# Kernel optimization log

Measured on AMD Instinct MI355X. Metric: run time of the kernel, lower is better.

Reference implementation:

```python
import jax, jax.numpy as jnp
import numpy as np

# SLAYER SRM-alpha neuron constants (standard slayerPytorch yaml defaults)
THETA = 10.0      # spike threshold
TAU_SR = 10.0     # synaptic response time constant
TAU_REF = 1.0     # refractory time constant
SCALE_REF = 2.0   # refractory scale (kernel amplitude = -scaleRef*theta)
TS = 1.0          # simulation timestep
K_LEN = 100       # SRM kernel truncation length (kernel is negligible beyond this)
A_REF = float(np.exp(-TS / TAU_REF))
# refractory alpha kernel ref[m] = K_REF * m * A_REF**m  (= -scaleRef*theta*(m*Ts/tauRef)*exp(1-m*Ts/tauRef))
K_REF = -SCALE_REF * THETA * float(np.e) * (TS / TAU_REF)


def _srm_kernel():
    # eps(t) = (t/tauSr) * exp(1 - t/tauSr), eps(0) = 0
    t = jnp.arange(K_LEN, dtype=jnp.float32) * TS
    return (t / TAU_SR) * jnp.exp(1.0 - t / TAU_SR)


def _psp(z):
    # z: (N, O, T). Causal FIR convolution in time with the SRM alpha kernel.
    N, O, T = z.shape
    k = _srm_kernel()[::-1].reshape(1, 1, K_LEN)  # flip: lax conv is correlation
    out = jax.lax.conv_general_dilated(z.reshape(N * O, 1, T), k,
                                       window_strides=(1,),
                                       padding=[(K_LEN - 1, 0)])
    return out.reshape(N, O, T)


def _refractory_and_spikes(u):
    # u: (T, N, O) post-synaptic potential. Sequential threshold + alpha refractory.
    # Alpha refractory kernel K*m*a^m is realized as a 2nd-order IIR over spikes:
    #   p[n] = a*p[n-1] + s[n]          (1st-order exp state)
    #   y[n] = a*(y[n-1] + K*p[n-1])    (refractory contribution at step n)
    def step(carry, u_t):
        p, y = carry
        y_n = A_REF * (y + K_REF * p)
        s = (u_t + y_n >= THETA).astype(u_t.dtype) / TS
        return (A_REF * p + s, y_n), (s, y_n)

    z0 = jnp.zeros(u.shape[1:], u.dtype)
    _, (s_seq, y_seq) = jax.lax.scan(step, (z0, z0), u)
    return s_seq, y_seq


def _layer(z):
    # slayer.spike(slayer.psp(fc(x)))
    u = _psp(z)
    s, _ = _refractory_and_spikes(jnp.moveaxis(u, -1, 0))
    return jnp.moveaxis(s, 0, -1)


def setup_inputs():
    key = jax.random.key(0)
    k1, k2, k3 = jax.random.split(key, 3)
    x = (jax.random.uniform(k1, (8, 2, 128, 128, 300)) < 0.03).astype(jnp.float32)
    # weight scales chosen so layer membranes hover around threshold -> realistic spiking
    w1 = jax.random.normal(k2, (410, 2 * 128 * 128), jnp.float32) * 0.01
    w2 = jax.random.normal(k3, (10, 410), jnp.float32) * 0.05
    return {"x": x, "w1": w1, "w2": w2}


def reference(x, w1, w2):
    N, T = x.shape[0], x.shape[-1]
    xf = x.reshape(N, -1, T)  # (N, C*H*W, T): slayer.dense is a full-spatial conv == GEMM per t
    s1 = _layer(jnp.einsum('nit,oi->not', xf, w1))  # fc1 -> psp -> spike, (N, 410, T)
    s2 = _layer(jnp.einsum('nit,oi->not', s1, w2))  # fc2 -> psp -> spike, (N, 10, T)
    return s2
```

## Files before the change

kernel.cpp:

```cpp
#include <hip/hip_runtime.h>

#define N_BATCH 8
#define I_DIM   32768
#define T_DIM   300
#define O1      410
#define O1P     416
#define O1Q     104
#define O2      10
#define KLEN    100
#define NCHUNK  16
#define NWORD   (I_DIM / 32)
#define CHCAP   128
#define NT      (N_BATCH * T_DIM)
#define GRP     4
#define NTG     (NT / GRP)

__global__ void transpose_w1_k(const float* __restrict__ w1, float* __restrict__ w1t) {
    __shared__ float tile[64][65];
    int i0 = blockIdx.x * 64;
    int o0 = blockIdx.y * 64;
    int tx = threadIdx.x & 63;
    int ty = threadIdx.x >> 6;
#pragma unroll
    for (int r = 0; r < 64; r += 4) {
        int o = o0 + r + ty;
        tile[r + ty][tx] = (o < O1) ? w1[(size_t)o * I_DIM + i0 + tx] : 0.0f;
    }
    __syncthreads();
#pragma unroll
    for (int r = 0; r < 64; r += 4) {
        int i = i0 + r + ty;
        int o = o0 + tx;
        if (o < O1P) w1t[(size_t)i * O1P + o] = (o < O1) ? tile[tx][r + ty] : 0.0f;
    }
}

__global__ __launch_bounds__(256) void bitmask_k(const float* __restrict__ x,
                                                 unsigned int* __restrict__ xb) {
    __shared__ float4 tile4[32 * 75];
    __shared__ unsigned int wbuf[300];
    int w   = blockIdx.x;
    int n   = blockIdx.y;
    int tid = threadIdx.x;
    const float4* src = (const float4*)(x + ((size_t)(n * I_DIM + w * 32)) * T_DIM);
    for (int q = tid; q < 32 * 75; q += 256) tile4[q] = src[q];
    __syncthreads();
    const float* tile = (const float*)tile4;
    int wv  = tid >> 6;
    int l   = tid & 63;
    int row = l & 31;
    int th  = l >> 5;
    for (int tp = wv; tp < 150; tp += 4) {
        int t = 2 * tp + th;
        float v = tile[row * 300 + t];
        unsigned long long m = __ballot(v != 0.0f);
        if (l == 0) {
            wbuf[2 * tp]     = (unsigned int)m;
            wbuf[2 * tp + 1] = (unsigned int)(m >> 32);
        }
    }
    __syncthreads();
    if (tid < 75) {
        uint4* dst = (uint4*)(xb + ((size_t)n * NWORD + w) * T_DIM);
        dst[tid] = ((const uint4*)wbuf)[tid];
    }
}

__device__ __forceinline__ void add4(float4& a, const float4 b) {
    a.x += b.x; a.y += b.y; a.z += b.z; a.w += b.w;
}

__global__ __launch_bounds__(512) void gather_partial_k(
        const float4* __restrict__ w1t4, const unsigned int* __restrict__ xb,
        float4* __restrict__ partial4) {
    int b     = blockIdx.x;
    int phase = b / (NTG * 8);
    int rem   = b - phase * (NTG * 8);
    int ntg   = rem >> 3;
    int k     = rem & 7;
    int chunk = phase * 8 + k;
    int nt0   = ntg * GRP;
    int tid   = threadIdx.x;
    int wv    = tid >> 6;
    int l     = tid & 63;

    __shared__ int s_idx[GRP][CHCAP];
    __shared__ int s_cnt[GRP];

    if ((wv & 1) == 0) {
        int g  = wv >> 1;
        int nt = nt0 + g;
        int n  = nt / T_DIM, t = nt - n * T_DIM;
        unsigned int word = xb[((size_t)n * NWORD + chunk * 64 + l) * T_DIM + t];
        int c   = __popc(word);
        int pfx = c;
#pragma unroll
        for (int d = 1; d < 64; d <<= 1) {
            int v = __shfl_up(pfx, d);
            if (l >= d) pfx += v;
        }
        pfx -= c;
        int base = chunk * 2048 + l * 32;
        while (word) {
            int bit = __ffs(word) - 1;
            if (pfx < CHCAP) s_idx[g][pfx] = base + bit;
            pfx++;
            word &= word - 1;
        }
        if (l == 63) s_cnt[g] = (pfx < CHCAP) ? pfx : CHCAP;
    }
    __syncthreads();

    int g  = tid >> 7;
    int oq = tid & 127;
    if (oq < O1Q) {
        const float4* wb = w1t4 + oq;
        int c = s_cnt[g];
        float4 z4 = make_float4(0.f, 0.f, 0.f, 0.f);
        float4 a0 = z4, a1 = z4, a2 = z4, a3 = z4;
        int j = 0;
        for (; j + 4 <= c; j += 4) {
            add4(a0, wb[(size_t)s_idx[g][j + 0] * O1Q]);
            add4(a1, wb[(size_t)s_idx[g][j + 1] * O1Q]);
            add4(a2, wb[(size_t)s_idx[g][j + 2] * O1Q]);
            add4(a3, wb[(size_t)s_idx[g][j + 3] * O1Q]);
        }
        for (; j < c; j++) add4(a0, wb[(size_t)s_idx[g][j] * O1Q]);
        add4(a0, a1); add4(a2, a3); add4(a0, a2);
        partial4[((size_t)(nt0 + g) * NCHUNK + chunk) * O1Q + oq] = a0;
    }
}

__global__ void reduce_k(const float* __restrict__ partial, float* __restrict__ up1) {
    int id = blockIdx.x * 256 + threadIdx.x;
    if (id >= NT * O1P) return;
    int nt = id / O1P;
    int o  = id - nt * O1P;
    float s = 0.0f;
    const float* p = partial + (size_t)nt * NCHUNK * O1P + o;
#pragma unroll
    for (int c = 0; c < NCHUNK; c++) s += p[c * O1P];
    if (o < O1) {
        int n = nt / T_DIM, t = nt - n * T_DIM;
        up1[((size_t)(n * O1 + o)) * T_DIM + t] = s;
    }
}

__global__ void psp_k(const float* __restrict__ z, float* __restrict__ u) {
    __shared__ float row[T_DIM];
    __shared__ float kern[KLEN];
    int r = blockIdx.x;
    int t = threadIdx.x;
    if (t < KLEN) {
        float a = (float)t / 10.0f;
        kern[t] = a * expf(1.0f - a);
    }
    if (t < T_DIM) row[t] = z[(size_t)r * T_DIM + t];
    __syncthreads();
    if (t < T_DIM) {
        float acc = 0.0f;
        int mmax = t < (KLEN - 1) ? t : (KLEN - 1);
        for (int m = 0; m <= mmax; m++) acc += kern[m] * row[t - m];
        u[(size_t)r * T_DIM + t] = acc;
    }
}

__global__ __launch_bounds__(64) void spike_tiled_k(const float* __restrict__ u,
                                                    float* __restrict__ s, int nrows) {
    __shared__ float lds[64][65];
    int r0 = blockIdx.x * 64;
    int l  = threadIdx.x;
    int tq = l & 15;
    int rb = l >> 4;
    const float A = 0.36787944117144233f;
    const float K = -54.365636569180904f;
    float p = 0.0f, y = 0.0f;

    for (int t0 = 0; t0 < T_DIM; t0 += 64) {
        int w = T_DIM - t0; if (w > 64) w = 64;
#pragma unroll
        for (int rep = 0; rep < 16; rep++) {
            int rr  = rep * 4 + rb;
            int row = r0 + rr;
            if (tq * 4 < w && row < nrows) {
                float4 v = *reinterpret_cast<const float4*>(
                    &u[(size_t)row * T_DIM + t0 + tq * 4]);
                lds[tq * 4 + 0][rr] = v.x; lds[tq * 4 + 1][rr] = v.y;
                lds[tq * 4 + 2][rr] = v.z; lds[tq * 4 + 3][rr] = v.w;
            }
        }
        __syncthreads();
        for (int tt = 0; tt < w; tt++) {
            float uv = lds[tt][l];
            y = A * (y + K * p);
            float sp = (uv + y >= 10.0f) ? 1.0f : 0.0f;
            p = A * p + sp;
            lds[tt][l] = sp;
        }
        __syncthreads();
#pragma unroll
        for (int rep = 0; rep < 16; rep++) {
            int rr  = rep * 4 + rb;
            int row = r0 + rr;
            if (tq * 4 < w && row < nrows) {
                float4 v;
                v.x = lds[tq * 4 + 0][rr]; v.y = lds[tq * 4 + 1][rr];
                v.z = lds[tq * 4 + 2][rr]; v.w = lds[tq * 4 + 3][rr];
                *reinterpret_cast<float4*>(&s[(size_t)row * T_DIM + t0 + tq * 4]) = v;
            }
        }
        __syncthreads();
    }
}

__global__ void gemm2_k(const float* __restrict__ s1, const float* __restrict__ w2,
                        float* __restrict__ up2) {
    int id = blockIdx.x * 256 + threadIdx.x;
    if (id >= N_BATCH * O2 * T_DIM) return;
    int t  = id % T_DIM;
    int o2 = (id / T_DIM) % O2;
    int n  = id / (T_DIM * O2);
    const float* s1n = s1 + (size_t)n * O1 * T_DIM + t;
    const float* w2r = w2 + o2 * O1;
    float a0 = 0, a1 = 0;
    for (int o = 0; o + 2 <= O1; o += 2) {
        a0 += w2r[o]     * s1n[(size_t)o * T_DIM];
        a1 += w2r[o + 1] * s1n[(size_t)(o + 1) * T_DIM];
    }
    up2[id] = a0 + a1;
}

extern "C" void kernel_launch(void* const* d_in, const int* in_sizes, int n_in,
                              void* d_out, int out_size, void* d_ws, size_t ws_size,
                              hipStream_t stream) {
    const float* x  = (const float*)d_in[0];
    const float* w1 = (const float*)d_in[1];
    const float* w2 = (const float*)d_in[2];
    float* out = (float*)d_out;

    char* ws = (char*)d_ws;
    float*        w1t     = (float*)ws;        ws += (size_t)I_DIM * O1P * 4;
    unsigned int* xb      = (unsigned int*)ws; ws += (size_t)N_BATCH * NWORD * T_DIM * 4;
    float*        partial = (float*)ws;        ws += (size_t)NT * NCHUNK * O1P * 4;
    float*        up1     = (float*)ws;        ws += (size_t)N_BATCH * O1 * T_DIM * 4;
    float*        u1      = (float*)ws;        ws += (size_t)N_BATCH * O1 * T_DIM * 4;
    float*        s1      = (float*)ws;        ws += (size_t)N_BATCH * O1 * T_DIM * 4;
    float*        up2     = (float*)ws;        ws += (size_t)N_BATCH * O2 * T_DIM * 4;
    float*        u2      = (float*)ws;

    transpose_w1_k<<<dim3(I_DIM / 64, (O1P + 63) / 64), 256, 0, stream>>>(w1, w1t);
    bitmask_k<<<dim3(NWORD, N_BATCH), 256, 0, stream>>>(x, xb);
    gather_partial_k<<<2 * NTG * 8, 512, 0, stream>>>((const float4*)w1t, xb,
                                                      (float4*)partial);
    reduce_k<<<(NT * O1P + 255) / 256, 256, 0, stream>>>(partial, up1);
    psp_k<<<N_BATCH * O1, 320, 0, stream>>>(up1, u1);
    spike_tiled_k<<<(N_BATCH * O1 + 63) / 64, 64, 0, stream>>>(u1, s1, N_BATCH * O1);
    gemm2_k<<<(N_BATCH * O2 * T_DIM + 255) / 256, 256, 0, stream>>>(s1, w2, up2);
    psp_k<<<N_BATCH * O2, 320, 0, stream>>>(up2, u2);
    spike_tiled_k<<<(N_BATCH * O2 + 63) / 64, 64, 0, stream>>>(u2, out, N_BATCH * O2);
}
```

Measured before the change: 409.1 us.

## Fuse PSP and spike kernels, restructure gemm2, add nontemporal loads/stores

Merges the PSP convolution and the sequential refractory/spike scan into one kernel that stages 16 neurons' time series in LDS, computes four outputs per thread with a register-shifted FIR, and has 16 threads run the scan. reduce_k now writes a contiguous (nt, o) layout so no transpose happens on write, and gemm2 computes all 10 outputs per thread using w2 cached in shared memory. Nontemporal hints are added to the large streaming loads and stores. This removes several launches and intermediate global round-trips, but the scan now runs on only 16 lanes per block with low parallelism.

```diff
diff --git a/kernel.cpp b/kernel.cpp
--- a/kernel.cpp
+++ b/kernel.cpp
@@ -14,6 +14,18 @@
 #define NT      (N_BATCH * T_DIM)
 #define GRP     4
 #define NTG     (NT / GRP)
+#define PSTRIDE 308
+
+typedef float nfloat4 __attribute__((ext_vector_type(4)));
+
+__device__ __forceinline__ float4 nt_load4(const float4* p) {
+    nfloat4 v = __builtin_nontemporal_load(reinterpret_cast<const nfloat4*>(p));
+    return make_float4(v.x, v.y, v.z, v.w);
+}
+__device__ __forceinline__ void nt_store4(float4* p, float4 v) {
+    nfloat4 w = {v.x, v.y, v.z, v.w};
+    __builtin_nontemporal_store(w, reinterpret_cast<nfloat4*>(p));
+}
 
 __global__ void transpose_w1_k(const float* __restrict__ w1, float* __restrict__ w1t) {
     __shared__ float tile[64][65];
@@ -24,7 +36,8 @@
 #pragma unroll
     for (int r = 0; r < 64; r += 4) {
         int o = o0 + r + ty;
-        tile[r + ty][tx] = (o < O1) ? w1[(size_t)o * I_DIM + i0 + tx] : 0.0f;
+        tile[r + ty][tx] = (o < O1) ? __builtin_nontemporal_load(&w1[(size_t)o * I_DIM + i0 + tx])
+                                    : 0.0f;
     }
     __syncthreads();
 #pragma unroll
@@ -43,7 +56,7 @@
     int n   = blockIdx.y;
     int tid = threadIdx.x;
     const float4* src = (const float4*)(x + ((size_t)(n * I_DIM + w * 32)) * T_DIM);
-    for (int q = tid; q < 32 * 75; q += 256) tile4[q] = src[q];
+    for (int q = tid; q < 32 * 75; q += 256) tile4[q] = nt_load4(&src[q]);
     __syncthreads();
     const float* tile = (const float*)tile4;
     int wv  = tid >> 6;
@@ -127,7 +140,7 @@
         }
         for (; j < c; j++) add4(a0, wb[(size_t)s_idx[g][j] * O1Q]);
         add4(a0, a1); add4(a2, a3); add4(a0, a2);
-        partial4[((size_t)(nt0 + g) * NCHUNK + chunk) * O1Q + oq] = a0;
+        nt_store4(&partial4[((size_t)(nt0 + g) * NCHUNK + chunk) * O1Q + oq], a0);
     }
 }
 
@@ -136,98 +149,118 @@
     if (id >= NT * O1P) return;
     int nt = id / O1P;
     int o  = id - nt * O1P;
+    const float* p = partial + (size_t)nt * NCHUNK * O1P + o;
     float s = 0.0f;
-    const float* p = partial + (size_t)nt * NCHUNK * O1P + o;
-#pragma unroll
-    for (int c = 0; c < NCHUNK; c++) s += p[c * O1P];
-    if (o < O1) {
-        int n = nt / T_DIM, t = nt - n * T_DIM;
-        up1[((size_t)(n * O1 + o)) * T_DIM + t] = s;
-    }
-}
-
-__global__ void psp_k(const float* __restrict__ z, float* __restrict__ u) {
-    __shared__ float row[T_DIM];
-    __shared__ float kern[KLEN];
-    int r = blockIdx.x;
-    int t = threadIdx.x;
-    if (t < KLEN) {
-        float a = (float)t / 10.0f;
-        kern[t] = a * expf(1.0f - a);
-    }
-    if (t < T_DIM) row[t] = z[(size_t)r * T_DIM + t];
-    __syncthreads();
-    if (t < T_DIM) {
-        float acc = 0.0f;
-        int mmax = t < (KLEN - 1) ? t : (KLEN - 1);
-        for (int m = 0; m <= mmax; m++) acc += kern[m] * row[t - m];
-        u[(size_t)r * T_DIM + t] = acc;
-    }
-}
-
-__global__ __launch_bounds__(64) void spike_tiled_k(const float* __restrict__ u,
-                                                    float* __restrict__ s, int nrows) {
-    __shared__ float lds[64][65];
-    int r0 = blockIdx.x * 64;
-    int l  = threadIdx.x;
-    int tq = l & 15;
-    int rb = l >> 4;
-    const float A = 0.36787944117144233f;
-    const float K = -54.365636569180904f;
-    float p = 0.0f, y = 0.0f;
-
-    for (int t0 = 0; t0 < T_DIM; t0 += 64) {
-        int w = T_DIM - t0; if (w > 64) w = 64;
-#pragma unroll
-        for (int rep = 0; rep < 16; rep++) {
-            int rr  = rep * 4 + rb;
-            int row = r0 + rr;
-            if (tq * 4 < w && row < nrows) {
-                float4 v = *reinterpret_cast<const float4*>(
-                    &u[(size_t)row * T_DIM + t0 + tq * 4]);
-                lds[tq * 4 + 0][rr] = v.x; lds[tq * 4 + 1][rr] = v.y;
-                lds[tq * 4 + 2][rr] = v.z; lds[tq * 4 + 3][rr] = v.w;
+#pragma unroll
+    for (int c = 0; c < NCHUNK; c++) s += __builtin_nontemporal_load(p + c * O1P);
+    up1[id] = s;
+}
+
+__global__ __launch_bounds__(256) void psp_spike_k(const float* __restrict__ up,
+                                                   float* __restrict__ s,
+                                                   int OP, int O) {
+    __shared__ float zrow[16 * PSTRIDE];
+    __shared__ float urow[16 * PSTRIDE];
+    __shared__ float kern[104];
+    int o0  = blockIdx.x * 16;
+    int n   = blockIdx.y;
+    int tid = threadIdx.x;
+
+    if (tid < 104) {
+        float a = (float)tid / 10.0f;
+        kern[tid] = (tid < KLEN) ? a * expf(1.0f - a) : 0.0f;
+    }
+    for (int idx = tid; idx < 16 * T_DIM; idx += 256) {
+        int t = idx >> 4, o = idx & 15;
+        zrow[o * PSTRIDE + t] = up[((size_t)n * T_DIM + t) * OP + o0 + o];
+    }
+    __syncthreads();
+    for (int task = tid; task < 16 * 75; task += 256) {
+        int o  = task & 15;
+        int t0 = (task >> 4) * 4;
+        const float* zr = &zrow[o * PSTRIDE];
+        float v0 = zr[t0], v1 = zr[t0 + 1], v2 = zr[t0 + 2], v3 = zr[t0 + 3];
+        float a0 = 0.f, a1 = 0.f, a2 = 0.f, a3 = 0.f;
+        for (int m = 0; m < KLEN; m++) {
+            float km = kern[m];
+            a0 += km * v0; a1 += km * v1; a2 += km * v2; a3 += km * v3;
+            v3 = v2; v2 = v1; v1 = v0;
+            int j = t0 - m - 1;
+            v0 = (j >= 0) ? zr[j] : 0.0f;
+        }
+        *reinterpret_cast<float4*>(&urow[o * PSTRIDE + t0]) = make_float4(a0, a1, a2, a3);
+    }
+    __syncthreads();
+    if (tid < 16) {
+        const float A = 0.36787944117144233f;
+        const float K = -54.365636569180904f;
+        float p = 0.0f, y = 0.0f;
+        float* ur = &urow[tid * PSTRIDE];
+        float* sr = &zrow[tid * PSTRIDE];
+        for (int t0 = 0; t0 < 296; t0 += 8) {
+            float4 ua = *(const float4*)&ur[t0];
+            float4 ub = *(const float4*)&ur[t0 + 4];
+            float uv[8] = {ua.x, ua.y, ua.z, ua.w, ub.x, ub.y, ub.z, ub.w};
+            float sp[8];
+#pragma unroll
+            for (int q = 0; q < 8; q++) {
+                y = A * (y + K * p);
+                float v = (uv[q] + y >= 10.0f) ? 1.0f : 0.0f;
+                p = A * p + v;
+                sp[q] = v;
             }
-        }
-        __syncthreads();
-        for (int tt = 0; tt < w; tt++) {
-            float uv = lds[tt][l];
-            y = A * (y + K * p);
-            float sp = (uv + y >= 10.0f) ? 1.0f : 0.0f;
-            p = A * p + sp;
-            lds[tt][l] = sp;
-        }
-        __syncthreads();
-#pragma unroll
-        for (int rep = 0; rep < 16; rep++) {
-            int rr  = rep * 4 + rb;
-            int row = r0 + rr;
-            if (tq * 4 < w && row < nrows) {
-                float4 v;
-                v.x = lds[tq * 4 + 0][rr]; v.y = lds[tq * 4 + 1][rr];
-                v.z = lds[tq * 4 + 2][rr]; v.w = lds[tq * 4 + 3][rr];
-                *reinterpret_cast<float4*>(&s[(size_t)row * T_DIM + t0 + tq * 4]) = v;
+            *(float4*)&sr[t0]     = make_float4(sp[0], sp[1], sp[2], sp[3]);
+            *(float4*)&sr[t0 + 4] = make_float4(sp[4], sp[5], sp[6], sp[7]);
+        }
+        {
+            float4 ua = *(const float4*)&ur[296];
+            float uv[4] = {ua.x, ua.y, ua.z, ua.w};
+            float sp[4];
+#pragma unroll
+            for (int q = 0; q < 4; q++) {
+                y = A * (y + K * p);
+                float v = (uv[q] + y >= 10.0f) ? 1.0f : 0.0f;
+                p = A * p + v;
+                sp[q] = v;
             }
-        }
-        __syncthreads();
-    }
-}
-
-__global__ void gemm2_k(const float* __restrict__ s1, const float* __restrict__ w2,
-                        float* __restrict__ up2) {
-    int id = blockIdx.x * 256 + threadIdx.x;
-    if (id >= N_BATCH * O2 * T_DIM) return;
-    int t  = id % T_DIM;
-    int o2 = (id / T_DIM) % O2;
-    int n  = id / (T_DIM * O2);
-    const float* s1n = s1 + (size_t)n * O1 * T_DIM + t;
-    const float* w2r = w2 + o2 * O1;
-    float a0 = 0, a1 = 0;
-    for (int o = 0; o + 2 <= O1; o += 2) {
-        a0 += w2r[o]     * s1n[(size_t)o * T_DIM];
-        a1 += w2r[o + 1] * s1n[(size_t)(o + 1) * T_DIM];
-    }
-    up2[id] = a0 + a1;
+            *(float4*)&sr[296] = make_float4(sp[0], sp[1], sp[2], sp[3]);
+        }
+    }
+    __syncthreads();
+    for (int task = tid; task < 16 * 75; task += 256) {
+        int o = task & 15, q = task >> 4;
+        int oo = o0 + o;
+        if (oo < O) {
+            float4 v = *(const float4*)&zrow[o * PSTRIDE + q * 4];
+            *reinterpret_cast<float4*>(&s[((size_t)n * O + oo) * T_DIM + q * 4]) = v;
+        }
+    }
+}
+
+__global__ __launch_bounds__(256) void gemm2_k(const float* __restrict__ s1,
+                                               const float* __restrict__ w2,
+                                               float* __restrict__ up2) {
+    __shared__ float w2s[O2 * O1];
+    int tid = threadIdx.x;
+    int nt  = blockIdx.x * 256 + tid;
+    for (int q = tid; q < O2 * O1; q += 256) w2s[q] = w2[q];
+    __syncthreads();
+    if (nt >= NT) return;
+    int n = nt / T_DIM, t = nt - n * T_DIM;
+    float acc[O2];
+#pragma unroll
+    for (int k = 0; k < O2; k++) acc[k] = 0.0f;
+    const float* sp = s1 + (size_t)n * O1 * T_DIM + t;
+    for (int o = 0; o < O1; o++) {
+        float v = sp[(size_t)o * T_DIM];
+#pragma unroll
+        for (int k = 0; k < O2; k++) acc[k] += w2s[k * O1 + o] * v;
+    }
+    float4* dst = (float4*)&up2[(size_t)nt * 16];
+    dst[0] = make_float4(acc[0], acc[1], acc[2], acc[3]);
+    dst[1] = make_float4(acc[4], acc[5], acc[6], acc[7]);
+    dst[2] = make_float4(acc[8], acc[9], 0.f, 0.f);
+    dst[3] = make_float4(0.f, 0.f, 0.f, 0.f);
 }
 
 extern "C" void kernel_launch(void* const* d_in, const int* in_sizes, int n_in,
@@ -242,20 +275,16 @@
     float*        w1t     = (float*)ws;        ws += (size_t)I_DIM * O1P * 4;
     unsigned int* xb      = (unsigned int*)ws; ws += (size_t)N_BATCH * NWORD * T_DIM * 4;
     float*        partial = (float*)ws;        ws += (size_t)NT * NCHUNK * O1P * 4;
-    float*        up1     = (float*)ws;        ws += (size_t)N_BATCH * O1 * T_DIM * 4;
-    float*        u1      = (float*)ws;        ws += (size_t)N_BATCH * O1 * T_DIM * 4;
+    float*        up1     = (float*)ws;        ws += (size_t)NT * O1P * 4;
     float*        s1      = (float*)ws;        ws += (size_t)N_BATCH * O1 * T_DIM * 4;
-    float*        up2     = (float*)ws;        ws += (size_t)N_BATCH * O2 * T_DIM * 4;
-    float*        u2      = (float*)ws;
+    float*        up2     = (float*)ws;
 
     transpose_w1_k<<<dim3(I_DIM / 64, (O1P + 63) / 64), 256, 0, stream>>>(w1, w1t);
     bitmask_k<<<dim3(NWORD, N_BATCH), 256, 0, stream>>>(x, xb);
     gather_partial_k<<<2 * NTG * 8, 512, 0, stream>>>((const float4*)w1t, xb,
                                                       (float4*)partial);
     reduce_k<<<(NT * O1P + 255) / 256, 256, 0, stream>>>(partial, up1);
-    psp_k<<<N_BATCH * O1, 320, 0, stream>>>(up1, u1);
-    spike_tiled_k<<<(N_BATCH * O1 + 63) / 64, 64, 0, stream>>>(u1, s1, N_BATCH * O1);
-    gemm2_k<<<(N_BATCH * O2 * T_DIM + 255) / 256, 256, 0, stream>>>(s1, w2, up2);
-    psp_k<<<N_BATCH * O2, 320, 0, stream>>>(up2, u2);
-    spike_tiled_k<<<(N_BATCH * O2 + 63) / 64, 64, 0, stream>>>(u2, out, N_BATCH * O2);
-}
+    psp_spike_k<<<dim3((O1 + 15) / 16, N_BATCH), 256, 0, stream>>>(up1, s1, O1P, O1);
+    gemm2_k<<<(NT + 255) / 256, 256, 0, stream>>>(s1, w2, up2);
+    psp_spike_k<<<dim3(1, N_BATCH), 256, 0, stream>>>(up2, out, 16, O2);
+}
```

Measured after the change: 367.0 us. 1.11x faster.
